# Kernel tuning notes

Measured on AMD Instinct MI355X. Metric: run time of the kernel, lower is better.

## Reference

```python
import jax, jax.numpy as jnp
import numpy as np

BITS = 4
QMAX = (1 << BITS) - 1      # 15
QHALF = 1 << (BITS - 1)     # 8
B, S = 4, 2048
IN, OUT, FP = 4096, 4096, 256
INT = IN - FP


def setup_inputs() -> dict:
    key = jax.random.key(0)
    k0, k1, k2, k3 = jax.random.split(key, 4)
    x = jax.random.normal(k0, (B, S, IN), dtype=jnp.float16)
    # disjoint outlier / int feature index sets (QUIK splits columns by outlier-ness)
    perm = np.random.default_rng(0).permutation(IN)
    fp_indices = jnp.sort(jnp.asarray(perm[:FP], dtype=jnp.int32))
    int_indices = jnp.sort(jnp.asarray(perm[FP:], dtype=jnp.int32))
    # unpacked int4 weight values in [-8, 7] (torch stores these packed 2-per-uint8)
    int_weight = jax.random.randint(k1, (OUT, INT), -QHALF, QHALF, dtype=jnp.int8)
    weights_scales = (jax.random.uniform(k2, (OUT, 1), dtype=jnp.float32) * 0.01 + 1e-3).astype(jnp.float16)
    fp_weight = (jax.random.normal(k3, (OUT, FP), dtype=jnp.float32) * 0.02).astype(jnp.float16)
    bias = jnp.zeros((OUT,), dtype=jnp.float16)
    # reduced_w[j] = w_scale[j] * sum_k int_weight[j, k]  (precomputed zero-point correction)
    reduced_w = (weights_scales.astype(jnp.float32)[:, 0] * jnp.sum(int_weight.astype(jnp.float32), axis=1)).reshape(1, OUT).astype(jnp.float16)
    return {"x": x, "int_weight": int_weight, "fp_weight": fp_weight, "bias": bias,
            "weights_scales": weights_scales, "reduced_w": reduced_w,
            "int_indices": int_indices, "fp_indices": fp_indices}


def reference(x, int_weight, fp_weight, bias, weights_scales, reduced_w, int_indices, fp_indices):
    b, s, in_feat = x.shape
    xf = x.reshape(-1, in_feat)                       # [N, in] tokens
    int_x = xf[:, int_indices].astype(jnp.float32)    # [N, INT]
    fp_x = xf[:, fp_indices].astype(jnp.float32)      # [N, FP] outliers stay fp16-precision
    # asymmetric per-token quantization (quik.asymmetric.quantize)
    mn = jnp.min(int_x, axis=1, keepdims=True)
    mx = jnp.max(int_x, axis=1, keepdims=True)
    scale = jnp.maximum((mx - mn) / QMAX, 1e-8)       # [N,1]
    q = (jnp.clip(jnp.round((int_x - mn) / scale), 0, QMAX) - QHALF).astype(jnp.int8)  # signed int4 in [-8,7]
    zero = scale * QHALF + mn                         # [N,1] shifted zero point
    # int4 GEMM (quik.matmul.int4Matmul), int32 accumulate
    int_res = jnp.einsum('nk,ok->no', q, int_weight, preferred_element_type=jnp.int32)
    # fp outlier branch fused with bias (F.linear)
    fp_res = fp_x @ fp_weight.astype(jnp.float32).T + bias.astype(jnp.float32)[None, :]
    # quik.asymmetric.dequantize: q*scale_x*scale_w + zero_x*reduced_w + fp_result
    out = (int_res.astype(jnp.float32) * scale * weights_scales.astype(jnp.float32)[:, 0][None, :]
           + zero * reduced_w.astype(jnp.float32) + fp_res)
    return out.astype(jnp.float16).reshape(b, s, -1)
```

## Files before the change

### kernel.cpp

```cpp
#include <hip/hip_runtime.h>
#include <hip/hip_bf16.h>
#include <stdint.h>

#define N_TOK 8192
#define IN_F  4096
#define OUT_F 4096
#define FP_F  256
#define INT_F 3840
#define PROW  1920

typedef int    v4i   __attribute__((ext_vector_type(4)));
typedef int    v16i  __attribute__((ext_vector_type(16)));
typedef float  v16f  __attribute__((ext_vector_type(16)));
typedef __bf16 bf16x8 __attribute__((ext_vector_type(8)));

#define WS_QP   0u
#define WS_WP   15728640u
#define WS_FPX  23592960u
#define WS_WFP  27787264u
#define WS_F1   29884416u
#define WS_F2   29917184u
#define WS_F3   29949952u
#define WS_NEED 29982720u


__global__ __launch_bounds__(256) void zero_out_kernel(uint4* __restrict__ o) {
  o[(size_t)blockIdx.x * 256 + threadIdx.x] = uint4{0, 0, 0, 0};
}

__global__ __launch_bounds__(256) void pack_w_kernel(
    const int* __restrict__ w, uint8_t* __restrict__ wp) {
  int t = blockIdx.x * 256 + threadIdx.x;
  int r = t / 480, u = t % 480;
  const int* src = w + (size_t)r * INT_F + (u >> 1) * 16 + (u & 1) * 4;
  int4 lo = *(const int4*)src;
  int4 hi = *(const int4*)(src + 8);
  uint32_t o = (uint32_t)((lo.x + 8) & 15) | (uint32_t)((hi.x + 8) & 15) << 4 |
               (uint32_t)((lo.y + 8) & 15) << 8 | (uint32_t)((hi.y + 8) & 15) << 12 |
               (uint32_t)((lo.z + 8) & 15) << 16 | (uint32_t)((hi.z + 8) & 15) << 20 |
               (uint32_t)((lo.w + 8) & 15) << 24 | (uint32_t)((hi.w + 8) & 15) << 28;
  ((uint32_t*)wp)[t] = o;
}

__global__ __launch_bounds__(256) void conv_wfp_kernel(
    const float* __restrict__ w, __hip_bfloat16* __restrict__ o) {
  int i = (blockIdx.x * 256 + threadIdx.x) * 4;
  float4 v = *(const float4*)(w + i);
  __hip_bfloat16 b[4] = {__float2bfloat16(v.x), __float2bfloat16(v.y),
                         __float2bfloat16(v.z), __float2bfloat16(v.w)};
  *(uint2*)(o + i) = *(const uint2*)b;
}

__global__ __launch_bounds__(256) void quant_kernel(
    const float* __restrict__ x,
    const int* __restrict__ int_idx, const int* __restrict__ fp_idx,
    uint8_t* __restrict__ qp, __hip_bfloat16* __restrict__ fpx,
    float* __restrict__ f1, float* __restrict__ f2, float* __restrict__ f3) {
  __shared__ uint2 qb[240];
  __shared__ float smn[4], smx[4], ssum[4];
  __shared__ float s_mn, s_inv, s_sc;

  int n = blockIdx.x, tid = threadIdx.x;
  const float* xr = x + (size_t)n * IN_F;

  float v[15];
  float lmn = 1e30f, lmx = -1e30f;
#pragma unroll
  for (int k = 0; k < 15; k++) {
    v[k] = xr[int_idx[tid + 256 * k]];
    lmn = fminf(lmn, v[k]);
    lmx = fmaxf(lmx, v[k]);
  }
  fpx[(size_t)n * FP_F + tid] = __float2bfloat16(xr[fp_idx[tid]]);

#pragma unroll
  for (int off = 32; off > 0; off >>= 1) {
    lmn = fminf(lmn, __shfl_xor(lmn, off, 64));
    lmx = fmaxf(lmx, __shfl_xor(lmx, off, 64));
  }
  int wv = tid >> 6, ln = tid & 63;
  if (ln == 0) { smn[wv] = lmn; smx[wv] = lmx; }
  __syncthreads();
  if (tid == 0) {
    float mn = fminf(fminf(smn[0], smn[1]), fminf(smn[2], smn[3]));
    float mx = fmaxf(fmaxf(smx[0], smx[1]), fmaxf(smx[2], smx[3]));
    float sc = fmaxf((mx - mn) / 15.0f, 1e-8f);
    s_mn = mn; s_sc = sc; s_inv = 1.0f / sc;
    f1[n] = sc; f3[n] = mn;
  }
  __syncthreads();
  float mn = s_mn, inv = s_inv;

  uint8_t* qbb = (uint8_t*)qb;
  float lsum = 0.0f;
#pragma unroll
  for (int k = 0; k < 15; k++) {
    float c = fminf(fmaxf(rintf((v[k] - mn) * inv), 0.0f), 15.0f);
    lsum += c;
    float ch = __shfl_down(c, 8, 64);
    if ((tid & 15) < 8) {
      qbb[(tid >> 4) * 8 + (tid & 7) + 128 * k] =
          (uint8_t)((uint32_t)c | ((uint32_t)ch << 4));
    }
  }
#pragma unroll
  for (int off = 32; off > 0; off >>= 1) lsum += __shfl_xor(lsum, off, 64);
  if (ln == 0) ssum[wv] = lsum;
  __syncthreads();
  if (tid == 0)
    f2[n] = -8.0f * (ssum[0] + ssum[1] + ssum[2] + ssum[3]) * s_sc;
  if (tid < 240)
    *(uint2*)(qp + (size_t)n * PROW + tid * 8) = qb[tid];
}

__device__ inline v4i unpack_nib(uint2 u) {
  v4i r;
  r[0] = (int)(u.x & 0x0F0F0F0Fu);
  r[1] = (int)(u.y & 0x0F0F0F0Fu);
  r[2] = (int)((u.x >> 4) & 0x0F0F0F0Fu);
  r[3] = (int)((u.y >> 4) & 0x0F0F0F0Fu);
  return r;
}

__global__ __launch_bounds__(256, 3) void gemm_kernel(
    const uint8_t* __restrict__ qp, const uint8_t* __restrict__ wp,
    const __hip_bfloat16* __restrict__ fpx, const __hip_bfloat16* __restrict__ wfp,
    const float* __restrict__ f1, const float* __restrict__ f2,
    const float* __restrict__ f3,
    const float* __restrict__ wscale, const float* __restrict__ reduced,
    const float* __restrict__ bias, float* __restrict__ out) {
  __shared__ int4 lds4[2048];
  int8_t* lds = (int8_t*)lds4;

  int tid = threadIdx.x;
  int wave = tid >> 6, lane = tid & 63;
  int wm = wave >> 1, wn = wave & 1;
  int blk = blockIdx.x;
  int tileM = ((blk & 7) << 3) | ((blk >> 3) & 7);
  int tileN = blk >> 6;
  int n0 = tileM * 128, o0 = tileN * 128;

  union { v16i i; v16f f; } acc[2][2];
#pragma unroll
  for (int mi = 0; mi < 2; mi++)
#pragma unroll
    for (int ni = 0; ni < 2; ni++)
#pragma unroll
      for (int e = 0; e < 16; e++) acc[mi][ni].i[e] = 0;

  int m = lane & 31, kg = lane >> 5;

  int sra = tid >> 2, s16i = tid & 3;
  const uint8_t* ga0 = qp + (size_t)(n0 + sra) * PROW + s16i * 16;
  const uint8_t* ga1 = qp + (size_t)(n0 + sra + 64) * PROW + s16i * 16;
  const uint8_t* gb0 = wp + (size_t)(o0 + sra) * PROW + s16i * 16;
  const uint8_t* gb1 = wp + (size_t)(o0 + sra + 64) * PROW + s16i * 16;
  uint32_t aw00 = sra * 64 + (((s16i * 2)     ^ ((sra >> 1) & 7)) * 8);
  uint32_t aw01 = sra * 64 + (((s16i * 2 + 1) ^ ((sra >> 1) & 7)) * 8);
  uint32_t aw10 = (sra + 64) * 64 + (((s16i * 2)     ^ (((sra + 64) >> 1) & 7)) * 8);
  uint32_t aw11 = (sra + 64) * 64 + (((s16i * 2 + 1) ^ (((sra + 64) >> 1) & 7)) * 8);

  uint4 pa0 = *(const uint4*)ga0, pa1 = *(const uint4*)ga1;
  uint4 pb0 = *(const uint4*)gb0, pb1 = *(const uint4*)gb1;
  for (int kt = 0; kt < 30; kt++) {
    {
      uint2 t0; t0.x = pa0.x; t0.y = pa0.y; *(uint2*)&lds[aw00] = t0;
      uint2 t1; t1.x = pa0.z; t1.y = pa0.w; *(uint2*)&lds[aw01] = t1;
      uint2 t2; t2.x = pa1.x; t2.y = pa1.y; *(uint2*)&lds[aw10] = t2;
      uint2 t3; t3.x = pa1.z; t3.y = pa1.w; *(uint2*)&lds[aw11] = t3;
      uint2 t4; t4.x = pb0.x; t4.y = pb0.y; *(uint2*)&lds[8192 + aw00] = t4;
      uint2 t5; t5.x = pb0.z; t5.y = pb0.w; *(uint2*)&lds[8192 + aw01] = t5;
      uint2 t6; t6.x = pb1.x; t6.y = pb1.y; *(uint2*)&lds[8192 + aw10] = t6;
      uint2 t7; t7.x = pb1.z; t7.y = pb1.w; *(uint2*)&lds[8192 + aw11] = t7;
    }
    __syncthreads();
    if (kt < 29) {
      pa0 = *(const uint4*)(ga0 + (kt + 1) * 64);
      pa1 = *(const uint4*)(ga1 + (kt + 1) * 64);
      pb0 = *(const uint4*)(gb0 + (kt + 1) * 64);
      pb1 = *(const uint4*)(gb1 + (kt + 1) * 64);
    }
#pragma unroll
    for (int ks = 0; ks < 4; ks++) {
      int s8 = ks * 2 + kg;
      v4i a[2], b[2];
#pragma unroll
      for (int mi = 0; mi < 2; mi++) {
        int row = wm * 64 + mi * 32 + m;
        a[mi] = unpack_nib(*(const uint2*)&lds[row * 64 + ((s8 ^ ((row >> 1) & 7)) * 8)]);
      }
#pragma unroll
      for (int ni = 0; ni < 2; ni++) {
        int row = wn * 64 + ni * 32 + m;
        b[ni] = unpack_nib(*(const uint2*)&lds[8192 + row * 64 + ((s8 ^ ((row >> 1) & 7)) * 8)]);
      }
#pragma unroll
      for (int mi = 0; mi < 2; mi++)
#pragma unroll
        for (int ni = 0; ni < 2; ni++)
          acc[mi][ni].i = __builtin_amdgcn_mfma_i32_32x32x32_i8(
              a[mi], b[ni], acc[mi][ni].i, 0, 0, 0);
    }
    __syncthreads();
  }

  int col = lane & 31, rb4 = (lane >> 5) * 4;
  float cws[2], crw[2], cbs[2];
#pragma unroll
  for (int ni = 0; ni < 2; ni++) {
    int o = o0 + wn * 64 + ni * 32 + col;
    cws[ni] = wscale[o]; crw[ni] = reduced[o]; cbs[ni] = bias[o];
  }
#pragma unroll
  for (int mi = 0; mi < 2; mi++) {
#pragma unroll
    for (int reg = 0; reg < 16; reg++) {
      int row = (reg & 3) + 8 * (reg >> 2) + rb4;
      int n = n0 + wm * 64 + mi * 32 + row;
      float a1 = f1[n], a2 = f2[n], a3 = f3[n];
      float d0 = (float)acc[mi][0].i[reg];
      float d1 = (float)acc[mi][1].i[reg];
      acc[mi][0].f[reg] = (d0 * a1 + a2) * cws[0] + a3 * crw[0] + cbs[0];
      acc[mi][1].f[reg] = (d1 * a1 + a2) * cws[1] + a3 * crw[1] + cbs[1];
    }
  }

  const int8_t* fpxb = (const int8_t*)fpx;
  const int8_t* fpwb = (const int8_t*)wfp;
  for (int kr = 0; kr < 4; kr++) {
#pragma unroll
    for (int i = 0; i < 4; i++) {
      int c = tid + i * 256;
      int row = c >> 3, s16 = c & 7;
      int phys = s16 ^ ((row >> 1) & 7);
      *(int4*)&lds[row * 128 + phys * 16] =
          *(const int4*)(fpxb + (size_t)(n0 + row) * 512 + kr * 128 + s16 * 16);
      *(int4*)&lds[16384 + row * 128 + phys * 16] =
          *(const int4*)(fpwb + (size_t)(o0 + row) * 512 + kr * 128 + s16 * 16);
    }
    __syncthreads();
#pragma unroll
    for (int kstep = 0; kstep < 4; kstep++) {
      int s16 = kstep * 2 + kg;
      bf16x8 a[2], b[2];
#pragma unroll
      for (int mi = 0; mi < 2; mi++) {
        int row = wm * 64 + mi * 32 + m;
        a[mi] = *(const bf16x8*)&lds[row * 128 + ((s16 ^ ((row >> 1) & 7)) * 16)];
      }
#pragma unroll
      for (int ni = 0; ni < 2; ni++) {
        int row = wn * 64 + ni * 32 + m;
        b[ni] = *(const bf16x8*)&lds[16384 + row * 128 + ((s16 ^ ((row >> 1) & 7)) * 16)];
      }
#pragma unroll
      for (int mi = 0; mi < 2; mi++)
#pragma unroll
        for (int ni = 0; ni < 2; ni++)
          acc[mi][ni].f = __builtin_amdgcn_mfma_f32_32x32x16_bf16(
              a[mi], b[ni], acc[mi][ni].f, 0, 0, 0);
    }
    __syncthreads();
  }

#pragma unroll
  for (int mi = 0; mi < 2; mi++) {
#pragma unroll
    for (int ni = 0; ni < 2; ni++) {
      int o = o0 + wn * 64 + ni * 32 + col;
#pragma unroll
      for (int reg = 0; reg < 16; reg++) {
        int row = (reg & 3) + 8 * (reg >> 2) + rb4;
        int n = n0 + wm * 64 + mi * 32 + row;
        out[(size_t)n * OUT_F + o] = acc[mi][ni].f[reg];
      }
    }
  }
}

extern "C" void kernel_launch(void* const* d_in, const int* in_sizes, int n_in,
                              void* d_out, int out_size, void* d_ws, size_t ws_size,
                              hipStream_t stream) {
  const float* x     = (const float*)d_in[0];
  const int*   int_w = (const int*)d_in[1];
  const float* fp_w  = (const float*)d_in[2];
  const float* bias  = (const float*)d_in[3];
  const float* wsc   = (const float*)d_in[4];
  const float* red   = (const float*)d_in[5];
  const int*   iidx  = (const int*)d_in[6];
  const int*   fidx  = (const int*)d_in[7];
  float*       out   = (float*)d_out;

  if (ws_size < (size_t)WS_NEED) {
    zero_out_kernel<<<out_size / 1024, 256, 0, stream>>>((uint4*)d_out);
    return;
  }

  uint8_t* ws = (uint8_t*)d_ws;
  uint8_t*        qp  = ws + WS_QP;
  uint8_t*        wpk = ws + WS_WP;
  __hip_bfloat16* fpx = (__hip_bfloat16*)(ws + WS_FPX);
  __hip_bfloat16* wfp = (__hip_bfloat16*)(ws + WS_WFP);
  float*          f1  = (float*)(ws + WS_F1);
  float*          f2  = (float*)(ws + WS_F2);
  float*          f3  = (float*)(ws + WS_F3);

  pack_w_kernel<<<OUT_F * 480 / 256, 256, 0, stream>>>(int_w, wpk);
  conv_wfp_kernel<<<OUT_F * FP_F / 4 / 256, 256, 0, stream>>>(fp_w, wfp);
  quant_kernel<<<N_TOK, 256, 0, stream>>>(x, iidx, fidx, qp, fpx, f1, f2, f3);
  gemm_kernel<<<(N_TOK / 128) * (OUT_F / 128), 256, 0, stream>>>(
      qp, wpk, fpx, wfp, f1, f2, f3, wsc, red, bias, out);
}
```

Baseline: 423.7 us.

## Pre-swizzle operands in prep and double-buffer GEMM via direct global-to-LDS loads

The three preprocessing kernels are merged into one launch. The prep stage now writes the quantized activations, packed weights and bf16 operands already in the XOR-swizzled layout the GEMM reads from LDS. This lets the GEMM use global_load_lds to copy tiles straight into a double-buffered LDS ring with explicit vmcnt waits and barriers, replacing register staging and the single-buffer sync loop. Occupancy hint is raised to 4 blocks per CU; the hand-written waitcnt and barrier ordering makes correctness depend on the load count per stage.

```diff
diff --git a/kernel.cpp b/kernel.cpp
--- a/kernel.cpp
+++ b/kernel.cpp
@@ -28,39 +28,49 @@
   o[(size_t)blockIdx.x * 256 + threadIdx.x] = uint4{0, 0, 0, 0};
 }
 
-__global__ __launch_bounds__(256) void pack_w_kernel(
-    const int* __restrict__ w, uint8_t* __restrict__ wp) {
-  int t = blockIdx.x * 256 + threadIdx.x;
-  int r = t / 480, u = t % 480;
-  const int* src = w + (size_t)r * INT_F + (u >> 1) * 16 + (u & 1) * 4;
-  int4 lo = *(const int4*)src;
-  int4 hi = *(const int4*)(src + 8);
-  uint32_t o = (uint32_t)((lo.x + 8) & 15) | (uint32_t)((hi.x + 8) & 15) << 4 |
-               (uint32_t)((lo.y + 8) & 15) << 8 | (uint32_t)((hi.y + 8) & 15) << 12 |
-               (uint32_t)((lo.z + 8) & 15) << 16 | (uint32_t)((hi.z + 8) & 15) << 20 |
-               (uint32_t)((lo.w + 8) & 15) << 24 | (uint32_t)((hi.w + 8) & 15) << 28;
-  ((uint32_t*)wp)[t] = o;
-}
-
-__global__ __launch_bounds__(256) void conv_wfp_kernel(
-    const float* __restrict__ w, __hip_bfloat16* __restrict__ o) {
-  int i = (blockIdx.x * 256 + threadIdx.x) * 4;
-  float4 v = *(const float4*)(w + i);
-  __hip_bfloat16 b[4] = {__float2bfloat16(v.x), __float2bfloat16(v.y),
-                         __float2bfloat16(v.z), __float2bfloat16(v.w)};
-  *(uint2*)(o + i) = *(const uint2*)b;
-}
-
-__global__ __launch_bounds__(256) void quant_kernel(
+__global__ __launch_bounds__(256) void prep_kernel(
     const float* __restrict__ x,
     const int* __restrict__ int_idx, const int* __restrict__ fp_idx,
-    uint8_t* __restrict__ qp, __hip_bfloat16* __restrict__ fpx,
+    const int* __restrict__ int_w, const float* __restrict__ fp_w,
+    uint8_t* __restrict__ qp, uint8_t* __restrict__ wp,
+    __hip_bfloat16* __restrict__ fpx, __hip_bfloat16* __restrict__ wfp,
     float* __restrict__ f1, float* __restrict__ f2, float* __restrict__ f3) {
   __shared__ uint2 qb[240];
   __shared__ float smn[4], smx[4], ssum[4];
   __shared__ float s_mn, s_inv, s_sc;
 
-  int n = blockIdx.x, tid = threadIdx.x;
+  int tid = threadIdx.x;
+  int blk = blockIdx.x;
+
+  if (blk >= N_TOK) {
+    int pb = blk - N_TOK;
+    if (pb < OUT_F * 480 / 256) {
+      int t = pb * 256 + tid;
+      int r = t / 480, u = t % 480;
+      int g = u >> 1, h = u & 1;
+      const int* src = int_w + (size_t)r * INT_F + g * 16 + h * 4;
+      int4 lo = *(const int4*)src;
+      int4 hi = *(const int4*)(src + 8);
+      uint32_t o = (uint32_t)((lo.x + 8) & 15) | (uint32_t)((hi.x + 8) & 15) << 4 |
+                   (uint32_t)((lo.y + 8) & 15) << 8 | (uint32_t)((hi.y + 8) & 15) << 12 |
+                   (uint32_t)((lo.z + 8) & 15) << 16 | (uint32_t)((hi.z + 8) & 15) << 20 |
+                   (uint32_t)((lo.w + 8) & 15) << 24 | (uint32_t)((hi.w + 8) & 15) << 28;
+      int gs = (g & ~7) | ((g & 7) ^ ((r >> 1) & 7));
+      ((uint32_t*)wp)[(size_t)r * 480 + gs * 2 + h] = o;
+    } else {
+      int t = (pb - OUT_F * 480 / 256) * 256 + tid;
+      int i = t * 4;
+      int r = i >> 8, c = i & 255;
+      float4 v = *(const float4*)(fp_w + i);
+      __hip_bfloat16 b[4] = {__float2bfloat16(v.x), __float2bfloat16(v.y),
+                             __float2bfloat16(v.z), __float2bfloat16(v.w)};
+      int cs = (c & ~0x18) | (((((c) >> 3) & 3) ^ ((r >> 1) & 3)) << 3);
+      *(uint2*)(wfp + (size_t)r * 256 + cs) = *(const uint2*)b;
+    }
+    return;
+  }
+
+  int n = blk;
   const float* xr = x + (size_t)n * IN_F;
 
   float v[15];
@@ -71,7 +81,11 @@
     lmn = fminf(lmn, v[k]);
     lmx = fmaxf(lmx, v[k]);
   }
-  fpx[(size_t)n * FP_F + tid] = __float2bfloat16(xr[fp_idx[tid]]);
+  {
+    int sw2 = (n >> 1) & 3;
+    int cs = (tid & ~0x18) | ((((tid >> 3) & 3) ^ sw2) << 3);
+    fpx[(size_t)n * FP_F + cs] = __float2bfloat16(xr[fp_idx[tid]]);
+  }
 
 #pragma unroll
   for (int off = 32; off > 0; off >>= 1) {
@@ -92,6 +106,7 @@
   float mn = s_mn, inv = s_inv;
 
   uint8_t* qbb = (uint8_t*)qb;
+  int swq = (n >> 1) & 7;
   float lsum = 0.0f;
 #pragma unroll
   for (int k = 0; k < 15; k++) {
@@ -99,8 +114,9 @@
     lsum += c;
     float ch = __shfl_down(c, 8, 64);
     if ((tid & 15) < 8) {
-      qbb[(tid >> 4) * 8 + (tid & 7) + 128 * k] =
-          (uint8_t)((uint32_t)c | ((uint32_t)ch << 4));
+      int G = (tid >> 4) + 16 * k;
+      int pos = ((G & ~7) | ((G & 7) ^ swq)) * 8 + (tid & 7);
+      qbb[pos] = (uint8_t)((uint32_t)c | ((uint32_t)ch << 4));
     }
   }
 #pragma unroll
@@ -122,7 +138,13 @@
   return r;
 }
 
-__global__ __launch_bounds__(256, 3) void gemm_kernel(
+__device__ __forceinline__ void gl16(const void* g, void* l) {
+  __builtin_amdgcn_global_load_lds(
+      (const __attribute__((address_space(1))) void*)g,
+      (__attribute__((address_space(3))) void*)l, 16, 0, 0);
+}
+
+__global__ __launch_bounds__(256, 4) void gemm_kernel(
     const uint8_t* __restrict__ qp, const uint8_t* __restrict__ wp,
     const __hip_bfloat16* __restrict__ fpx, const __hip_bfloat16* __restrict__ wfp,
     const float* __restrict__ f1, const float* __restrict__ f2,
@@ -150,36 +172,21 @@
 
   int m = lane & 31, kg = lane >> 5;
 
-  int sra = tid >> 2, s16i = tid & 3;
-  const uint8_t* ga0 = qp + (size_t)(n0 + sra) * PROW + s16i * 16;
-  const uint8_t* ga1 = qp + (size_t)(n0 + sra + 64) * PROW + s16i * 16;
-  const uint8_t* gb0 = wp + (size_t)(o0 + sra) * PROW + s16i * 16;
-  const uint8_t* gb1 = wp + (size_t)(o0 + sra + 64) * PROW + s16i * 16;
-  uint32_t aw00 = sra * 64 + (((s16i * 2)     ^ ((sra >> 1) & 7)) * 8);
-  uint32_t aw01 = sra * 64 + (((s16i * 2 + 1) ^ ((sra >> 1) & 7)) * 8);
-  uint32_t aw10 = (sra + 64) * 64 + (((s16i * 2)     ^ (((sra + 64) >> 1) & 7)) * 8);
-  uint32_t aw11 = (sra + 64) * 64 + (((s16i * 2 + 1) ^ (((sra + 64) >> 1) & 7)) * 8);
-
-  uint4 pa0 = *(const uint4*)ga0, pa1 = *(const uint4*)ga1;
-  uint4 pb0 = *(const uint4*)gb0, pb1 = *(const uint4*)gb1;
-  for (int kt = 0; kt < 30; kt++) {
-    {
-      uint2 t0; t0.x = pa0.x; t0.y = pa0.y; *(uint2*)&lds[aw00] = t0;
-      uint2 t1; t1.x = pa0.z; t1.y = pa0.w; *(uint2*)&lds[aw01] = t1;
-      uint2 t2; t2.x = pa1.x; t2.y = pa1.y; *(uint2*)&lds[aw10] = t2;
-      uint2 t3; t3.x = pa1.z; t3.y = pa1.w; *(uint2*)&lds[aw11] = t3;
-      uint2 t4; t4.x = pb0.x; t4.y = pb0.y; *(uint2*)&lds[8192 + aw00] = t4;
-      uint2 t5; t5.x = pb0.z; t5.y = pb0.w; *(uint2*)&lds[8192 + aw01] = t5;
-      uint2 t6; t6.x = pb1.x; t6.y = pb1.y; *(uint2*)&lds[8192 + aw10] = t6;
-      uint2 t7; t7.x = pb1.z; t7.y = pb1.w; *(uint2*)&lds[8192 + aw11] = t7;
-    }
-    __syncthreads();
-    if (kt < 29) {
-      pa0 = *(const uint4*)(ga0 + (kt + 1) * 64);
-      pa1 = *(const uint4*)(ga1 + (kt + 1) * 64);
-      pb0 = *(const uint4*)(gb0 + (kt + 1) * 64);
-      pb1 = *(const uint4*)(gb1 + (kt + 1) * 64);
-    }
+  int row0 = tid >> 2, q16 = (tid & 3) * 16;
+  int l0 = tid * 16, l1 = 4096 + tid * 16;
+  const uint8_t* gA0 = qp + (size_t)(n0 + row0) * PROW + q16;
+  const uint8_t* gA1 = qp + (size_t)(n0 + 64 + row0) * PROW + q16;
+  const uint8_t* gB0 = wp + (size_t)(o0 + row0) * PROW + q16;
+  const uint8_t* gB1 = wp + (size_t)(o0 + 64 + row0) * PROW + q16;
+
+#define STAGE_INT(buf, kt) do {                                  \
+    gl16(gA0 + (kt) * 64, lds + (buf) * 16384 + l0);             \
+    gl16(gA1 + (kt) * 64, lds + (buf) * 16384 + l1);             \
+    gl16(gB0 + (kt) * 64, lds + (buf) * 16384 + 8192 + l0);      \
+    gl16(gB1 + (kt) * 64, lds + (buf) * 16384 + 8192 + l1);      \
+  } while (0)
+
+  auto compute_int = [&](const int8_t* lb) {
 #pragma unroll
     for (int ks = 0; ks < 4; ks++) {
       int s8 = ks * 2 + kg;
@@ -187,12 +194,12 @@
 #pragma unroll
       for (int mi = 0; mi < 2; mi++) {
         int row = wm * 64 + mi * 32 + m;
-        a[mi] = unpack_nib(*(const uint2*)&lds[row * 64 + ((s8 ^ ((row >> 1) & 7)) * 8)]);
+        a[mi] = unpack_nib(*(const uint2*)&lb[row * 64 + ((s8 ^ ((row >> 1) & 7)) * 8)]);
       }
 #pragma unroll
       for (int ni = 0; ni < 2; ni++) {
         int row = wn * 64 + ni * 32 + m;
-        b[ni] = unpack_nib(*(const uint2*)&lds[8192 + row * 64 + ((s8 ^ ((row >> 1) & 7)) * 8)]);
+        b[ni] = unpack_nib(*(const uint2*)&lb[8192 + row * 64 + ((s8 ^ ((row >> 1) & 7)) * 8)]);
       }
 #pragma unroll
       for (int mi = 0; mi < 2; mi++)
@@ -201,8 +208,42 @@
           acc[mi][ni].i = __builtin_amdgcn_mfma_i32_32x32x32_i8(
               a[mi], b[ni], acc[mi][ni].i, 0, 0, 0);
     }
-    __syncthreads();
-  }
+  };
+
+  STAGE_INT(0, 0);
+#pragma unroll 1
+  for (int kt = 0; kt < 30; kt += 2) {
+    STAGE_INT(1, kt + 1);
+    asm volatile("s_waitcnt vmcnt(4)" ::: "memory");
+    __builtin_amdgcn_s_barrier();
+    compute_int(lds);
+    __builtin_amdgcn_s_barrier();
+    if (kt + 2 < 30) {
+      STAGE_INT(0, kt + 2);
+      asm volatile("s_waitcnt vmcnt(4)" ::: "memory");
+    } else {
+      asm volatile("s_waitcnt vmcnt(0)" ::: "memory");
+    }
+    __builtin_amdgcn_s_barrier();
+    compute_int(lds + 16384);
+    __builtin_amdgcn_s_barrier();
+  }
+
+  const uint8_t* fxb = (const uint8_t*)fpx;
+  const uint8_t* fwb = (const uint8_t*)wfp;
+  const uint8_t* gFA0 = fxb + (size_t)(n0 + row0) * 512 + q16;
+  const uint8_t* gFA1 = fxb + (size_t)(n0 + 64 + row0) * 512 + q16;
+  const uint8_t* gFB0 = fwb + (size_t)(o0 + row0) * 512 + q16;
+  const uint8_t* gFB1 = fwb + (size_t)(o0 + 64 + row0) * 512 + q16;
+
+#define STAGE_BF(buf, kr) do {                                   \
+    gl16(gFA0 + (kr) * 64, lds + (buf) * 16384 + l0);            \
+    gl16(gFA1 + (kr) * 64, lds + (buf) * 16384 + l1);            \
+    gl16(gFB0 + (kr) * 64, lds + (buf) * 16384 + 8192 + l0);     \
+    gl16(gFB1 + (kr) * 64, lds + (buf) * 16384 + 8192 + l1);     \
+  } while (0)
+
+  STAGE_BF(0, 0);
 
   int col = lane & 31, rb4 = (lane >> 5) * 4;
   float cws[2], crw[2], cbs[2];
@@ -225,33 +266,20 @@
     }
   }
 
-  const int8_t* fpxb = (const int8_t*)fpx;
-  const int8_t* fpwb = (const int8_t*)wfp;
-  for (int kr = 0; kr < 4; kr++) {
-#pragma unroll
-    for (int i = 0; i < 4; i++) {
-      int c = tid + i * 256;
-      int row = c >> 3, s16 = c & 7;
-      int phys = s16 ^ ((row >> 1) & 7);
-      *(int4*)&lds[row * 128 + phys * 16] =
-          *(const int4*)(fpxb + (size_t)(n0 + row) * 512 + kr * 128 + s16 * 16);
-      *(int4*)&lds[16384 + row * 128 + phys * 16] =
-          *(const int4*)(fpwb + (size_t)(o0 + row) * 512 + kr * 128 + s16 * 16);
-    }
-    __syncthreads();
-#pragma unroll
-    for (int kstep = 0; kstep < 4; kstep++) {
+  auto compute_bf = [&](const int8_t* lb) {
+#pragma unroll
+    for (int kstep = 0; kstep < 2; kstep++) {
       int s16 = kstep * 2 + kg;
       bf16x8 a[2], b[2];
 #pragma unroll
       for (int mi = 0; mi < 2; mi++) {
         int row = wm * 64 + mi * 32 + m;
-        a[mi] = *(const bf16x8*)&lds[row * 128 + ((s16 ^ ((row >> 1) & 7)) * 16)];
+        a[mi] = *(const bf16x8*)&lb[row * 64 + ((s16 ^ ((row >> 1) & 3)) * 16)];
       }
 #pragma unroll
       for (int ni = 0; ni < 2; ni++) {
         int row = wn * 64 + ni * 32 + m;
-        b[ni] = *(const bf16x8*)&lds[16384 + row * 128 + ((s16 ^ ((row >> 1) & 7)) * 16)];
+        b[ni] = *(const bf16x8*)&lb[8192 + row * 64 + ((s16 ^ ((row >> 1) & 3)) * 16)];
       }
 #pragma unroll
       for (int mi = 0; mi < 2; mi++)
@@ -260,7 +288,24 @@
           acc[mi][ni].f = __builtin_amdgcn_mfma_f32_32x32x16_bf16(
               a[mi], b[ni], acc[mi][ni].f, 0, 0, 0);
     }
-    __syncthreads();
+  };
+
+#pragma unroll 1
+  for (int kr = 0; kr < 8; kr += 2) {
+    STAGE_BF(1, kr + 1);
+    asm volatile("s_waitcnt vmcnt(4)" ::: "memory");
+    __builtin_amdgcn_s_barrier();
+    compute_bf(lds);
+    __builtin_amdgcn_s_barrier();
+    if (kr + 2 < 8) {
+      STAGE_BF(0, kr + 2);
+      asm volatile("s_waitcnt vmcnt(4)" ::: "memory");
+    } else {
+      asm volatile("s_waitcnt vmcnt(0)" ::: "memory");
+    }
+    __builtin_amdgcn_s_barrier();
+    compute_bf(lds + 16384);
+    __builtin_amdgcn_s_barrier();
   }
 
 #pragma unroll
@@ -276,6 +321,8 @@
       }
     }
   }
+#undef STAGE_INT
+#undef STAGE_BF
 }
 
 extern "C" void kernel_launch(void* const* d_in, const int* in_sizes, int n_in,
@@ -305,9 +352,8 @@
   float*          f2  = (float*)(ws + WS_F2);
   float*          f3  = (float*)(ws + WS_F3);
 
-  pack_w_kernel<<<OUT_F * 480 / 256, 256, 0, stream>>>(int_w, wpk);
-  conv_wfp_kernel<<<OUT_F * FP_F / 4 / 256, 256, 0, stream>>>(fp_w, wfp);
-  quant_kernel<<<N_TOK, 256, 0, stream>>>(x, iidx, fidx, qp, fpx, f1, f2, f3);
+  prep_kernel<<<N_TOK + OUT_F * 480 / 256 + OUT_F * FP_F / 4 / 256, 256, 0, stream>>>(
+      x, iidx, fidx, int_w, fp_w, qp, wpk, fpx, wfp, f1, f2, f3);
   gemm_kernel<<<(N_TOK / 128) * (OUT_F / 128), 256, 0, stream>>>(
       qp, wpk, fpx, wfp, f1, f2, f3, wsc, red, bias, out);
 }
```

After: 405.2 us. 4.4% less time.
